# Optimization experiments

Hardware: AMD Instinct MI355X
Metric: run time of the kernel (lower is better)

Reference implementation:

```python
import jax, jax.numpy as jnp
import numpy as np

B, N, C, D, UP, KNN, MULT, PH = 4, 2048, 256, 64, 4, 20, 4, 64
EPS = 1e-5


def conv1d(x, w, b):
    # x: (B, Cin, N), w: (Cout, Cin)
    return jnp.einsum('oc,bcn->bon', w, x) + b[None, :, None]


def conv2d(x, w, b):
    # x: (B, Cin, N, K), 1x1 conv
    return jnp.einsum('oc,bcnk->bonk', w, x) + b[None, :, None, None]


def bn2d(x, g, bt, rm, rv):
    # eval-mode BatchNorm2d with running stats
    inv = jax.lax.rsqrt(rv + EPS)
    return g[None, :, None, None] * (x - rm[None, :, None, None]) * inv[None, :, None, None] + bt[None, :, None, None]


def group(f, idx):
    # f: (B, C, N), idx: (B, N, K) -> (B, C, N, K)
    return jax.vmap(lambda fb, ib: fb[:, ib])(f, idx)


def setup_inputs() -> dict:
    k0 = jax.random.key(0)
    ks = iter(jax.random.split(k0, 48))
    nx = lambda: next(ks)
    rn = lambda shape, s=0.05: jax.random.normal(nx(), shape, dtype=jnp.float32) * s
    z = lambda n: jnp.zeros((n,), jnp.float32)
    o = lambda n: jnp.ones((n,), jnp.float32)
    inp = {
        'pos': jax.random.normal(nx(), (B, 3, N), dtype=jnp.float32),
        'key': jax.random.normal(nx(), (B, C, N), dtype=jnp.float32),
        'query': jax.random.normal(nx(), (B, C, N), dtype=jnp.float32),
        # MLP_Res (mlp_v): in_dim=2C, hidden=C, out=C
        'wv1': rn((C, 2 * C)), 'bv1': z(C),
        'wv2': rn((C, C)), 'bv2': z(C),
        'wvs': rn((C, 2 * C)), 'bvs': z(C),
        # key/query/value projections to dim D
        'wk': rn((D, C)), 'bk': z(D),
        'wq': rn((D, C)), 'bq': z(D),
        'wval': rn((D, C)), 'bval': z(D),
        # pos_mlp: Conv2d(3,PH) -> BN -> ReLU -> Conv2d(PH,D)
        'pw1': rn((PH, 3)), 'pb1': z(PH), 'pg': o(PH), 'pbt': z(PH), 'prm': z(PH), 'prv': o(PH),
        'pw2': rn((D, PH)), 'pb2': z(D),
        # attn_mlp: Conv2d(D, D*MULT) -> BN -> ReLU -> ConvTranspose2d(D*MULT, D, (UP,1), (UP,1))
        'aw1': rn((D * MULT, D)), 'ab1': z(D * MULT), 'ag': o(D * MULT), 'abt': z(D * MULT), 'arm': z(D * MULT), 'arv': o(D * MULT),
        'ctw': rn((D * MULT, D, UP)), 'ctb': z(D),
        # conv_end: Conv1d(D, C)
        'we': rn((C, D)), 'be': z(C),
    }
    return inp


def reference(pos, key, query, wv1, bv1, wv2, bv2, wvs, bvs, wk, bk, wq, bq, wval, bval,
              pw1, pb1, pg, pbt, prm, prv, pw2, pb2,
              aw1, ab1, ag, abt, arm, arv, ctw, ctb, we, be):
    # mlp_v (MLP_Res) on concat([key, query])
    x = jnp.concatenate([key, query], axis=1)  # (B, 2C, N)
    value = conv1d(jax.nn.relu(conv1d(x, wv1, bv1)), wv2, bv2) + conv1d(x, wvs, bvs)  # (B, C, N)
    identity = value

    k_f = conv1d(key, wk, bk)      # (B, D, N)
    q_f = conv1d(query, wq, bq)    # (B, D, N)
    v_f = conv1d(value, wval, bval)

    # KNN (include_self=True): smallest-KNN indices of pairwise sq distance
    p = jnp.transpose(pos, (0, 2, 1))  # (B, N, 3)
    sq = jnp.sum(p * p, axis=-1)
    dist = sq[:, :, None] + sq[:, None, :] - 2.0 * jnp.einsum('bnc,bmc->bnm', p, p)
    idx = jax.lax.top_k(-dist, KNN)[1]  # (B, N, KNN)

    k_g = group(k_f, idx)                              # (B, D, N, KNN)
    qk_rel = q_f[:, :, :, None] - k_g
    pos_rel = pos[:, :, :, None] - group(pos, idx)     # (B, 3, N, KNN)

    h = jax.nn.relu(bn2d(conv2d(pos_rel, pw1, pb1), pg, pbt, prm, prv))
    pos_emb = conv2d(h, pw2, pb2)                      # (B, D, N, KNN)

    a = jax.nn.relu(bn2d(conv2d(qk_rel + pos_emb, aw1, ab1), ag, abt, arm, arv))  # (B, D*MULT, N, KNN)
    # ConvTranspose2d with kernel=(UP,1), stride=(UP,1): non-overlapping, out[b,o,n*UP+r,k]
    ct = jnp.einsum('bcnk,cor->bornk', a, ctw)         # (B, D, UP, N, KNN)
    Bv = a.shape[0]
    ct = jnp.transpose(ct, (0, 1, 3, 2, 4)).reshape(Bv, D, N * UP, KNN) + ctb[None, :, None, None]
    attn = jax.nn.softmax(ct, axis=-1)                 # softmax over neighbors

    v_g = group(v_f, idx) + pos_emb                    # (B, D, N, KNN)
    v_up = jnp.repeat(v_g, UP, axis=2)                 # nearest Upsample (UP,1)
    agg = jnp.sum(attn * v_up, axis=-1)                # (B, D, N*UP)
    y = conv1d(agg, we, be)                            # (B, C, N*UP)
    return y + jnp.repeat(identity, UP, axis=2)
```

## Files before the change

kernel.cpp:

```cpp
#include <hip/hip_runtime.h>
#include <hip/hip_bf16.h>

#define Bq 4
#define Nq 2048
#define Cq 256
#define Dq 64
#define UPq 4
#define KNNq 20
#define PHq 64
#define DMq 256
#define PTS 16

typedef __attribute__((ext_vector_type(8))) short short8;
typedef __attribute__((ext_vector_type(4))) short short4v;
typedef __attribute__((ext_vector_type(4))) float f32x4;
typedef __hip_bfloat16 bf16;

__device__ __forceinline__ void ld16(float* d, const float* s){
  *reinterpret_cast<float4*>(d) = *reinterpret_cast<const float4*>(s);
}
__device__ __forceinline__ unsigned short f2b(float x){
  bf16 h = __float2bfloat16(x);
  return *reinterpret_cast<unsigned short*>(&h);
}
__device__ __forceinline__ float b2f(short s){
  return __bfloat162float(*reinterpret_cast<bf16*>(&s));
}

__device__ __forceinline__ void swz(const float* __restrict__ src,
                                    short* __restrict__ dst,
                                    int M, int K, int g, bool transp)
{
  int j = g & 7, lane = (g >> 3) & 63, rest = g >> 9;
  int KS = K >> 5;
  int ks = rest % KS, mt = rest / KS;
  int m = mt*16 + (lane & 15);
  int k = ks*32 + ((lane >> 4) << 3) + j;
  float v = transp ? src[k*M + m] : src[m*K + k];
  dst[g] = (short)f2b(v);
}

__device__ __forceinline__ void swz_s(const float* __restrict__ src,
                                      short* __restrict__ dst,
                                      int M, int K, int g,
                                      const float* __restrict__ gam,
                                      const float* __restrict__ var)
{
  int j = g & 7, lane = (g >> 3) & 63, rest = g >> 9;
  int KS = K >> 5;
  int ks = rest % KS, mt = rest / KS;
  int m = mt*16 + (lane & 15);
  int k = ks*32 + ((lane >> 4) << 3) + j;
  float sc = gam[m] * rsqrtf(var[m] + 1e-5f);
  dst[g] = (short)f2b(src[m*K + k] * sc);
}

__global__ __launch_bounds__(256) void k_prep(
    const float* __restrict__ aw1, const float* __restrict__ ctw,
    const float* __restrict__ wv1, const float* __restrict__ wvs,
    const float* __restrict__ wv2, const float* __restrict__ wk,
    const float* __restrict__ wq,  const float* __restrict__ wval,
    const float* __restrict__ pw2, const float* __restrict__ we,
    short* __restrict__ aw1b, short* __restrict__ ctwT,
    short* __restrict__ wv1b, short* __restrict__ wvsb,
    short* __restrict__ wv2b, short* __restrict__ wkb,
    short* __restrict__ wqb,  short* __restrict__ wvalb,
    short* __restrict__ pw2b, short* __restrict__ web,
    const float* __restrict__ ag, const float* __restrict__ arv)
{
  const int t = threadIdx.x, bidx = blockIdx.x;
  if (bidx < 512){
    swz(wv1, wv1b, 256, 512, bidx*256 + t, false);
  } else if (bidx < 1024){
    swz(wvs, wvsb, 256, 512, (bidx-512)*256 + t, false);
  } else if (bidx < 1280){
    swz(wv2, wv2b, 256, 256, (bidx-1024)*256 + t, false);
  } else if (bidx < 1344){
    swz(wk, wkb, 64, 256, (bidx-1280)*256 + t, false);
  } else if (bidx < 1408){
    swz(wq, wqb, 64, 256, (bidx-1344)*256 + t, false);
  } else if (bidx < 1472){
    swz(wval, wvalb, 64, 256, (bidx-1408)*256 + t, false);
  } else if (bidx < 1488){
    swz(pw2, pw2b, 64, 64, (bidx-1472)*256 + t, false);
  } else if (bidx < 1552){
    swz_s(aw1, aw1b, 256, 64, (bidx-1488)*256 + t, ag, arv);
  } else if (bidx < 1616){
    swz(we, web, 256, 64, (bidx-1552)*256 + t, false);
  } else {
    swz(ctw, ctwT, 256, 256, (bidx-1616)*256 + t, true);
  }
}

__global__ __launch_bounds__(256) void k_value(
    const float* __restrict__ key, const float* __restrict__ query,
    const short* __restrict__ wv1b, const short* __restrict__ wvsb,
    const short* __restrict__ wv2b, const short* __restrict__ wkb,
    const short* __restrict__ wqb,  const short* __restrict__ wvalb,
    const float* __restrict__ bv1, const float* __restrict__ bv2,
    const float* __restrict__ bvs, const float* __restrict__ bk,
    const float* __restrict__ bq,  const float* __restrict__ bval,
    float* __restrict__ valueT, short* __restrict__ kfT,
    short* __restrict__ qfT,    short* __restrict__ vfT)
{
  __shared__ __align__(16) short Xb[16*520];
  __shared__ __align__(16) short hidB[16*264];
  __shared__ __align__(16) short valB[16*264];
  __shared__ __align__(16) float valF[16*264];
  const int t = threadIdx.x;
  const int b = blockIdx.x >> 7;
  const int n0 = (blockIdx.x & 127) * PTS;
  const int lane = t & 63, quad = lane >> 4, l15 = lane & 15, w = t >> 6;

  {
    const int c4 = t >> 2, pq = t & 3;
    #pragma unroll
    for (int pass=0; pass<4; pass++){
      int c = pass*64 + c4;
      float4 kv = *reinterpret_cast<const float4*>(key   + ((size_t)(b*Cq+c))*Nq + n0 + pq*4);
      float4 qv = *reinterpret_cast<const float4*>(query + ((size_t)(b*Cq+c))*Nq + n0 + pq*4);
      const float* kf_ = (const float*)&kv;
      const float* qf_ = (const float*)&qv;
      #pragma unroll
      for (int i=0;i<4;i++){
        Xb[(pq*4+i)*520 + c]       = (short)f2b(kf_[i]);
        Xb[(pq*4+i)*520 + 256 + c] = (short)f2b(qf_[i]);
      }
    }
  }
  __syncthreads();

  f32x4 acc1[4], accS[4];
  #pragma unroll
  for (int jm=0;jm<4;jm++){ acc1[jm]=(f32x4)0.f; accS[jm]=(f32x4)0.f; }

  #pragma unroll
  for (int ks=0;ks<16;ks++){
    const int kcol = ks*32 + quad*8;
    short8 xb = *reinterpret_cast<const short8*>(&Xb[l15*520 + kcol]);
    #pragma unroll
    for (int jm=0;jm<4;jm++){
      int mt = w*4 + jm;
      short8 a1 = *reinterpret_cast<const short8*>(wv1b + ((mt*16+ks)*64 + lane)*8);
      short8 as = *reinterpret_cast<const short8*>(wvsb + ((mt*16+ks)*64 + lane)*8);
      acc1[jm] = __builtin_amdgcn_mfma_f32_16x16x32_bf16(a1, xb, acc1[jm], 0,0,0);
      accS[jm] = __builtin_amdgcn_mfma_f32_16x16x32_bf16(as, xb, accS[jm], 0,0,0);
    }
  }
  #pragma unroll
  for (int jm=0;jm<4;jm++){
    #pragma unroll
    for (int r=0;r<4;r++){
      int h = (w*4+jm)*16 + quad*4 + r;
      hidB[l15*264 + h] = (short)f2b(fmaxf(acc1[jm][r] + bv1[h], 0.f));
    }
  }
  __syncthreads();

  #pragma unroll
  for (int ks=0;ks<8;ks++){
    const int kcol = ks*32 + quad*8;
    short8 hb = *reinterpret_cast<const short8*>(&hidB[l15*264 + kcol]);
    #pragma unroll
    for (int jm=0;jm<4;jm++){
      int mt = w*4 + jm;
      short8 a = *reinterpret_cast<const short8*>(wv2b + ((mt*8+ks)*64 + lane)*8);
      accS[jm] = __builtin_amdgcn_mfma_f32_16x16x32_bf16(a, hb, accS[jm], 0,0,0);
    }
  }
  #pragma unroll
  for (int jm=0;jm<4;jm++){
    #pragma unroll
    for (int r=0;r<4;r++){
      int c = (w*4+jm)*16 + quad*4 + r;
      float v = accS[jm][r] + bv2[c] + bvs[c];
      valF[l15*264 + c] = v;
      valB[l15*264 + c] = (short)f2b(v);
    }
  }
  __syncthreads();

  #pragma unroll
  for (int p=0;p<PTS;p++)
    valueT[((size_t)(b*Nq + n0 + p))*Cq + t] = valF[p*264 + t];

  {
    f32x4 pk4=(f32x4)0.f, pq4=(f32x4)0.f, pv4=(f32x4)0.f;
    #pragma unroll
    for (int ks=0;ks<8;ks++){
      const int kcol = ks*32 + quad*8;
      short8 xk = *reinterpret_cast<const short8*>(&Xb[l15*520 + kcol]);
      short8 xq = *reinterpret_cast<const short8*>(&Xb[l15*520 + 256 + kcol]);
      short8 xv = *reinterpret_cast<const short8*>(&valB[l15*264 + kcol]);
      short8 ak = *reinterpret_cast<const short8*>(wkb  + ((w*8+ks)*64 + lane)*8);
      short8 aq = *reinterpret_cast<const short8*>(wqb  + ((w*8+ks)*64 + lane)*8);
      short8 av = *reinterpret_cast<const short8*>(wvalb+ ((w*8+ks)*64 + lane)*8);
      pk4 = __builtin_amdgcn_mfma_f32_16x16x32_bf16(ak, xk, pk4, 0,0,0);
      pq4 = __builtin_amdgcn_mfma_f32_16x16x32_bf16(aq, xq, pq4, 0,0,0);
      pv4 = __builtin_amdgcn_mfma_f32_16x16x32_bf16(av, xv, pv4, 0,0,0);
    }
    short4v ok, oq, ov;
    #pragma unroll
    for (int r=0;r<4;r++){
      int o = w*16 + quad*4 + r;
      ok[r] = (short)f2b(pk4[r] + bk[o]);
      oq[r] = (short)f2b(pq4[r] + bq[o]);
      ov[r] = (short)f2b(pv4[r] + bval[o]);
    }
    int n = n0 + l15;
    size_t base = ((size_t)(b*Nq+n))*Dq + w*16 + quad*4;
    *reinterpret_cast<short4v*>(kfT + base) = ok;
    *reinterpret_cast<short4v*>(qfT + base) = oq;
    *reinterpret_cast<short4v*>(vfT + base) = ov;
  }
}

__global__ __launch_bounds__(256) void k_knn(const float* __restrict__ pos,
                                             int* __restrict__ idxT)
{
  const int t = threadIdx.x;
  const int lane = t & 63;
  const int w = t >> 6;
  const int pid = blockIdx.x*4 + w;
  const int b = pid >> 11;
  const int n = pid & (Nq-1);
  const float* px = pos + (size_t)(b*3+0)*Nq;
  const float* py = pos + (size_t)(b*3+1)*Nq;
  const float* pz = pos + (size_t)(b*3+2)*Nq;
  const float xn=px[n], yn=py[n], zn=pz[n];
  const float sqn = __fadd_rn(__fadd_rn(__fmul_rn(xn,xn),__fmul_rn(yn,yn)),__fmul_rn(zn,zn));

  double kd[32];
  #pragma unroll
  for (int i=0;i<32;i++){
    int j = i*64 + lane;
    float x=px[j], y=py[j], z=pz[j];
    float sqj = __fadd_rn(__fadd_rn(__fmul_rn(x,x),__fmul_rn(y,y)),__fmul_rn(z,z));
    float dot = __fadd_rn(__fadd_rn(__fmul_rn(xn,x),__fmul_rn(yn,y)),__fmul_rn(zn,z));
    float d   = __fsub_rn(__fadd_rn(sqn,sqj), __fmul_rn(2.0f,dot));
    unsigned u = __float_as_uint(d);
    u ^= ((unsigned)((int)u >> 31)) | 0x80000000u;
    kd[i] = (double)u * 2048.0 + (double)j;
  }

  const double BIG = 9.0e15;
  double last = -1.0;
  for (int s=0;s<KNNq;s++){
    double c[16];
    #pragma unroll
    for (int i=0;i<16;i++){
      double a0 = (kd[i]    > last) ? kd[i]    : BIG;
      double a1 = (kd[i+16] > last) ? kd[i+16] : BIG;
      c[i] = fmin(a0, a1);
    }
    #pragma unroll
    for (int off=8; off>0; off>>=1){
      #pragma unroll
      for (int i=0;i<off;i++) c[i] = fmin(c[i], c[i+off]);
    }
    double m = c[0];
    #pragma unroll
    for (int off=1; off<64; off<<=1)
      m = fmin(m, __shfl_xor(m, off));
    if (lane == 0){
      unsigned long long kk = (unsigned long long)m;
      idxT[(size_t)pid*KNNq + s] = (int)(kk & 2047ull);
    }
    last = m;
  }
}

#define UADDR(row, colb) ((((row)*128 + (colb)) ^ (((row)&7)<<4)))
#define SADDR(row, colb) ((((row)*256 + (colb)) ^ (((row)&7)<<4)))

__global__ __launch_bounds__(256, 4) void k_attn(
  const float* __restrict__ pos,
  const float* __restrict__ valueT, const short* __restrict__ kfT,
  const short* __restrict__ qfT,    const short* __restrict__ vfT,
  const int* __restrict__ idxT,
  const float* __restrict__ pw1, const float* __restrict__ pb1,
  const float* __restrict__ pg,  const float* __restrict__ pbt,
  const float* __restrict__ prm, const float* __restrict__ prv,
  const short* __restrict__ pw2b, const float* __restrict__ pb2,
  const short* __restrict__ aw1b, const float* __restrict__ ab1,
  const float* __restrict__ ag,  const float* __restrict__ abt,
  const float* __restrict__ arm, const float* __restrict__ arv,
  const short* __restrict__ ctwT,
  const short* __restrict__ web,  const float* __restrict__ be,
  float* __restrict__ out)
{
  __shared__ __align__(16) char unionA[22528];
  __shared__ __align__(16) char unionB[6144];
  __shared__ __align__(16) char unionC[6144];
  __shared__ __align__(16) short vgB[64*40];

  float* sh2S = (float*)(unionA + 12288);
  float* prl  = (float*)unionC;
  int*   nb   = (int*)(unionC + 576);

  const int t = threadIdx.x;
  const int b  = blockIdx.x >> 10;
  const int n0 = (blockIdx.x & 1023) * 2;
  const int lane = t & 63, quad = lane >> 4, l15 = lane & 15, w = t >> 6;
  const size_t bN = (size_t)b * Nq;
  const int obase = w*16 + quad*4;

  if (t < 48){
    int p = (t >= 24);
    int k = t - p*24;
    int nn = n0 + p;
    int j = (k < KNNq) ? idxT[(bN + nn)*KNNq + k] : nn;
    nb[t] = j;
    #pragma unroll
    for (int d=0; d<3; d++){
      prl[d*48+t] = pos[((size_t)(b*3+d))*Nq + nn] - pos[((size_t)(b*3+d))*Nq + j];
    }
  }
  {
    float sc = ag[t] * rsqrtf(arv[t] + 1e-5f);
    sh2S[t]  = ab1[t]*sc + (abt[t] - arm[t]*sc);
  }
  __syncthreads();

  short4v pq4[3], pk4[3], pv4[3];
  #pragma unroll
  for (int nt=0; nt<3; nt++){
    int pk = nt*16 + l15;
    int p  = (pk >= 24);
    int j  = nb[pk];
    pq4[nt] = *reinterpret_cast<const short4v*>(qfT + (bN + n0 + p)*Dq + obase);
    pk4[nt] = *reinterpret_cast<const short4v*>(kfT + (bN + j)*Dq + obase);
    pv4[nt] = *reinterpret_cast<const short4v*>(vfT + (bN + j)*Dq + obase);
  }

  {
    const int ph = t & 63;
    float sc = pg[ph] * rsqrtf(prv[ph] + 1e-5f);
    float w0 = pw1[ph*3+0]*sc, w1 = pw1[ph*3+1]*sc, w2 = pw1[ph*3+2]*sc;
    float bb = pb1[ph]*sc + (pbt[ph] - prm[ph]*sc);
    #pragma unroll
    for (int m=0;m<12;m++){
      int pk = w + m*4;
      float h = fmaf(w0, prl[pk], fmaf(w1, prl[48+pk], fmaf(w2, prl[96+pk], bb)));
      *(short*)(unionB + UADDR(pk, ph*2)) = (short)f2b(fmaxf(h, 0.f));
    }
  }
  __syncthreads();

  {
    f32x4 accP[3];
    #pragma unroll
    for (int nt=0;nt<3;nt++) accP[nt]=(f32x4)0.f;
    #pragma unroll
    for (int ks=0;ks<2;ks++){
      const int kcolb = (ks*32 + quad*8)*2;
      short8 a = *reinterpret_cast<const short8*>(pw2b + ((w*2+ks)*64 + lane)*8);
      #pragma unroll
      for (int nt=0;nt<3;nt++){
        short8 bb = *reinterpret_cast<const short8*>(unionB + UADDR(nt*16+l15, kcolb));
        accP[nt] = __builtin_amdgcn_mfma_f32_16x16x32_bf16(a, bb, accP[nt], 0,0,0);
      }
    }
    #pragma unroll
    for (int nt=0;nt<3;nt++){
      int pk = nt*16 + l15;
      bool vld = (pk < 20) || (pk >= 24 && pk < 44);
      int col  = pk - (pk >= 24 ? 4 : 0);
      short4v ut4;
      #pragma unroll
      for (int r=0;r<4;r++){
        int o = obase + r;
        float pe = accP[nt][r] + pb2[o];
        ut4[r] = (short)f2b((b2f(pq4[nt][r]) - b2f(pk4[nt][r])) + pe);
        if (vld) vgB[o*40 + col] = (short)f2b(b2f(pv4[nt][r]) + pe);
      }
      *(short4v*)(unionC + UADDR(pk, obase*2)) = ut4;
    }
  }
  __syncthreads();

  f32x4 accT[4][3];
  #pragma unroll
  for (int jm=0;jm<4;jm++)
    #pragma unroll
    for (int nt=0;nt<3;nt++) accT[jm][nt]=(f32x4)0.f;

  #pragma unroll
  for (int ch=0; ch<2; ch++){
    f32x4 accC[2][3];
    #pragma unroll
    for (int jm=0;jm<2;jm++)
      #pragma unroll
      for (int nt=0;nt<3;nt++) accC[jm][nt]=(f32x4)0.f;
    #pragma unroll
    for (int ks=0;ks<2;ks++){
      const int kcolb = (ks*32 + quad*8)*2;
      short8 bb[3];
      #pragma unroll
      for (int nt=0;nt<3;nt++)
        bb[nt] = *reinterpret_cast<const short8*>(unionC + UADDR(nt*16+l15, kcolb));
      #pragma unroll
      for (int jm=0;jm<2;jm++){
        int mt = ch*8 + w*2 + jm;
        short8 a = *reinterpret_cast<const short8*>(aw1b + ((mt*2+ks)*64 + lane)*8);
        #pragma unroll
        for (int nt=0;nt<3;nt++)
          accC[jm][nt] = __builtin_amdgcn_mfma_f32_16x16x32_bf16(a, bb[nt], accC[jm][nt], 0,0,0);
      }
    }
    if (ch == 1) __syncthreads();
    #pragma unroll
    for (int jm=0;jm<2;jm++){
      const int colb = ((w*2+jm)*16 + quad*4)*2;
      #pragma unroll
      for (int nt=0;nt<3;nt++){
        int pk = nt*16 + l15;
        short4v pkv;
        #pragma unroll
        for (int r=0;r<4;r++){
          int c = ch*128 + (w*2+jm)*16 + quad*4 + r;
          pkv[r] = (short)f2b(fmaxf(accC[jm][nt][r] + sh2S[c], 0.f));
        }
        *(short4v*)(unionA + SADDR(pk, colb)) = pkv;
      }
    }
    __syncthreads();
    #pragma unroll
    for (int ksl=0; ksl<4; ksl++){
      const int kcolb = (ksl*32 + quad*8)*2;
      short8 bb[3];
      #pragma unroll
      for (int nt=0;nt<3;nt++)
        bb[nt] = *reinterpret_cast<const short8*>(unionA + SADDR(nt*16+l15, kcolb));
      #pragma unroll
      for (int jm=0;jm<4;jm++){
        int mt = w*4 + jm;
        short8 a = *reinterpret_cast<const short8*>(ctwT + ((mt*8 + ch*4 + ksl)*64 + lane)*8);
        #pragma unroll
        for (int nt=0;nt<3;nt++)
          accT[jm][nt] = __builtin_amdgcn_mfma_f32_16x16x32_bf16(a, bb[nt], accT[jm][nt], 0,0,0);
      }
    }
  }
  __syncthreads();

  #pragma unroll
  for (int nt=0;nt<3;nt++){
    int pk = nt*16 + l15;
    bool vld = (pk < 20) || (pk >= 24 && pk < 44);
    int col  = pk - (pk >= 24 ? 4 : 0);
    if (vld){
      #pragma unroll
      for (int jm=0;jm<4;jm++){
        #pragma unroll
        for (int r=0;r<4;r++){
          int row = (w*4+jm)*16 + quad*4 + r;
          *(short*)(unionA + row*88 + col*2) = (short)f2b(accT[jm][nt][r]);
        }
      }
    }
  }
  __syncthreads();

  float4 idv[4];
  if (l15 < 8){
    int p = l15 >> 2;
    #pragma unroll
    for (int jm=0;jm<4;jm++)
      idv[jm] = *reinterpret_cast<const float4*>(valueT + (bN + n0 + p)*Cq + (w*4+jm)*16 + quad*4);
  }
  {
    const int o = t >> 2, rr = t & 3;
    #pragma unroll
    for (int p=0;p<2;p++){
      float ct[20];
      #pragma unroll
      for (int q=0;q<5;q++){
        short4v cv = *reinterpret_cast<const short4v*>(unionA + t*88 + p*40 + q*8);
        #pragma unroll
        for (int i=0;i<4;i++) ct[q*4+i] = b2f(cv[i]);
      }
      float m = ct[0];
      #pragma unroll
      for (int k=1;k<20;k++) m = fmaxf(m, ct[k]);
      float s = 0.f, a = 0.f;
      #pragma unroll
      for (int q=0;q<5;q++){
        short4v vv = *reinterpret_cast<const short4v*>((const char*)vgB + o*80 + p*40 + q*8);
        #pragma unroll
        for (int i=0;i<4;i++){
          float e = __expf(ct[q*4+i] - m);
          s += e;
          a = fmaf(e, b2f(vv[i]), a);
        }
      }
      *(short*)(unionB + UADDR(p*4+rr, o*2)) = (short)f2b(__fdividef(a, s));
    }
  }
  __syncthreads();

  {
    f32x4 accE[4];
    #pragma unroll
    for (int jm=0;jm<4;jm++) accE[jm]=(f32x4)0.f;
    #pragma unroll
    for (int ks=0;ks<2;ks++){
      const int kcolb = (ks*32 + quad*8)*2;
      short8 bb = *reinterpret_cast<const short8*>(unionB + UADDR(l15, kcolb));
      #pragma unroll
      for (int jm=0;jm<4;jm++){
        int mt = w*4 + jm;
        short8 a = *reinterpret_cast<const short8*>(web + ((mt*2+ks)*64 + lane)*8);
        accE[jm] = __builtin_amdgcn_mfma_f32_16x16x32_bf16(a, bb, accE[jm], 0,0,0);
      }
    }
    if (l15 < 8){
      int p = l15 >> 2, rr = l15 & 3;
      #pragma unroll
      for (int jm=0;jm<4;jm++){
        float4 b4 = *reinterpret_cast<const float4*>(be + (w*4+jm)*16 + quad*4);
        #pragma unroll
        for (int r=0;r<4;r++){
          int c = (w*4+jm)*16 + quad*4 + r;
          float y = accE[jm][r] + ((const float*)&b4)[r] + ((const float*)&idv[jm])[r];
          out[((size_t)(b*Cq+c))*((size_t)Nq*UPq) + (size_t)(n0+p)*UPq + rr] = y;
        }
      }
    }
  }
}

extern "C" void kernel_launch(void* const* d_in, const int* in_sizes, int n_in,
                              void* d_out, int out_size, void* d_ws, size_t ws_size,
                              hipStream_t stream)
{
  const float* pos  = (const float*)d_in[0];
  const float* key  = (const float*)d_in[1];
  const float* qry  = (const float*)d_in[2];
  const float* wv1  = (const float*)d_in[3];
  const float* bv1  = (const float*)d_in[4];
  const float* wv2  = (const float*)d_in[5];
  const float* bv2  = (const float*)d_in[6];
  const float* wvs  = (const float*)d_in[7];
  const float* bvs  = (const float*)d_in[8];
  const float* wk   = (const float*)d_in[9];
  const float* bk   = (const float*)d_in[10];
  const float* wq   = (const float*)d_in[11];
  const float* bq   = (const float*)d_in[12];
  const float* wval = (const float*)d_in[13];
  const float* bval = (const float*)d_in[14];
  const float* pw1  = (const float*)d_in[15];
  const float* pb1  = (const float*)d_in[16];
  const float* pg   = (const float*)d_in[17];
  const float* pbt  = (const float*)d_in[18];
  const float* prm  = (const float*)d_in[19];
  const float* prv  = (const float*)d_in[20];
  const float* pw2  = (const float*)d_in[21];
  const float* pb2  = (const float*)d_in[22];
  const float* aw1  = (const float*)d_in[23];
  const float* ab1  = (const float*)d_in[24];
  const float* ag   = (const float*)d_in[25];
  const float* abt  = (const float*)d_in[26];
  const float* arm  = (const float*)d_in[27];
  const float* arv  = (const float*)d_in[28];
  const float* ctw  = (const float*)d_in[29];
  const float* we   = (const float*)d_in[31];
  const float* be   = (const float*)d_in[32];

  char* ws = (char*)d_ws;
  float* valueT = (float*)(ws);
  short* kfT    = (short*)(ws + 8388608);
  short* qfT    = (short*)(ws + 9437184);
  short* vfT    = (short*)(ws + 10485760);
  int*   idxT   = (int*)  (ws + 11534336);
  short* aw1b   = (short*)(ws + 12189696);
  short* ctwT   = (short*)(ws + 12222464);
  short* wv1b   = (short*)(ws + 12353536);
  short* wvsb   = (short*)(ws + 12615680);
  short* wv2b   = (short*)(ws + 12877824);
  short* wkb    = (short*)(ws + 13008896);
  short* wqb    = (short*)(ws + 13041664);
  short* wvalb  = (short*)(ws + 13074432);
  short* pw2b   = (short*)(ws + 13107200);
  short* web    = (short*)(ws + 13115392);
  float* out    = (float*)d_out;

  k_prep<<<dim3(1872), dim3(256), 0, stream>>>(
      aw1, ctw, wv1, wvs, wv2, wk, wq, wval, pw2, we,
      aw1b, ctwT, wv1b, wvsb, wv2b, wkb, wqb, wvalb, pw2b, web,
      ag, arv);
  k_value<<<dim3(Bq*Nq/PTS), dim3(256), 0, stream>>>(
      key, qry, wv1b, wvsb, wv2b, wkb, wqb, wvalb,
      bv1, bv2, bvs, bk, bq, bval,
      valueT, kfT, qfT, vfT);
  k_knn<<<dim3(Bq*Nq/4), dim3(256), 0, stream>>>(pos, idxT);
  k_attn<<<dim3(Bq*Nq/2), dim3(256), 0, stream>>>(
      pos, valueT, kfT, qfT, vfT, idxT,
      pw1, pb1, pg, pbt, prm, prv, pw2b, pb2,
      aw1b, ab1, ag, abt, arm, arv, ctwT, web, be, out);
}
```

Before: 285.3 us.

## Process four points per attention block with 512 threads to widen MFMA tiles

The attention kernel now handles four query points per block with eight waves instead of two points with four waves. Shared buffers double in size and the warp-to-tile mapping changes so each wave covers six neighbor tiles in the attn_mlp GEMMs. This is meant to reuse each loaded weight fragment across more neighbor columns and to halve the block count. The cost is more shared memory and registers per block, which can lower occupancy, and a launch_bounds of (512,4) that may be hard to satisfy.

```diff
diff --git a/kernel.cpp b/kernel.cpp
--- a/kernel.cpp
+++ b/kernel.cpp
@@ -16,9 +16,6 @@
 typedef __attribute__((ext_vector_type(4))) float f32x4;
 typedef __hip_bfloat16 bf16;
 
-__device__ __forceinline__ void ld16(float* d, const float* s){
-  *reinterpret_cast<float4*>(d) = *reinterpret_cast<const float4*>(s);
-}
 __device__ __forceinline__ unsigned short f2b(float x){
   bf16 h = __float2bfloat16(x);
   return *reinterpret_cast<unsigned short*>(&h);
@@ -273,7 +270,7 @@
 #define UADDR(row, colb) ((((row)*128 + (colb)) ^ (((row)&7)<<4)))
 #define SADDR(row, colb) ((((row)*256 + (colb)) ^ (((row)&7)<<4)))
 
-__global__ __launch_bounds__(256, 4) void k_attn(
+__global__ __launch_bounds__(512, 4) void k_attn(
   const float* __restrict__ pos,
   const float* __restrict__ valueT, const short* __restrict__ kfT,
   const short* __restrict__ qfT,    const short* __restrict__ vfT,
@@ -289,34 +286,36 @@
   const short* __restrict__ web,  const float* __restrict__ be,
   float* __restrict__ out)
 {
-  __shared__ __align__(16) char unionA[22528];
-  __shared__ __align__(16) char unionB[6144];
-  __shared__ __align__(16) char unionC[6144];
-  __shared__ __align__(16) short vgB[64*40];
-
-  float* sh2S = (float*)(unionA + 12288);
+  __shared__ __align__(16) char unionA[43008];
+  __shared__ __align__(16) char unionB[12288];
+  __shared__ __align__(16) char unionC[12288];
+  __shared__ __align__(16) short vgB[64*84];
+
+  float* sh2S = (float*)(unionA + 24576);
   float* prl  = (float*)unionC;
-  int*   nb   = (int*)(unionC + 576);
+  int*   nb   = (int*)(unionC + 1152);
 
   const int t = threadIdx.x;
-  const int b  = blockIdx.x >> 10;
-  const int n0 = (blockIdx.x & 1023) * 2;
+  const int b  = blockIdx.x >> 9;
+  const int n0 = (blockIdx.x & 511) * 4;
   const int lane = t & 63, quad = lane >> 4, l15 = lane & 15, w = t >> 6;
   const size_t bN = (size_t)b * Nq;
-  const int obase = w*16 + quad*4;
-
-  if (t < 48){
-    int p = (t >= 24);
+  const int wm = w & 3;
+  const int ntb = (w >> 2) * 3;
+  const int obase2 = wm*16 + quad*4;
+
+  if (t < 96){
+    int p = (t*683) >> 14;
     int k = t - p*24;
     int nn = n0 + p;
     int j = (k < KNNq) ? idxT[(bN + nn)*KNNq + k] : nn;
     nb[t] = j;
     #pragma unroll
     for (int d=0; d<3; d++){
-      prl[d*48+t] = pos[((size_t)(b*3+d))*Nq + nn] - pos[((size_t)(b*3+d))*Nq + j];
-    }
-  }
-  {
+      prl[d*96+t] = pos[((size_t)(b*3+d))*Nq + nn] - pos[((size_t)(b*3+d))*Nq + j];
+    }
+  }
+  if (t < 256){
     float sc = ag[t] * rsqrtf(arv[t] + 1e-5f);
     sh2S[t]  = ab1[t]*sc + (abt[t] - arm[t]*sc);
   }
@@ -325,12 +324,12 @@
   short4v pq4[3], pk4[3], pv4[3];
   #pragma unroll
   for (int nt=0; nt<3; nt++){
-    int pk = nt*16 + l15;
-    int p  = (pk >= 24);
+    int pk = (ntb+nt)*16 + l15;
+    int p  = (pk*683) >> 14;
     int j  = nb[pk];
-    pq4[nt] = *reinterpret_cast<const short4v*>(qfT + (bN + n0 + p)*Dq + obase);
-    pk4[nt] = *reinterpret_cast<const short4v*>(kfT + (bN + j)*Dq + obase);
-    pv4[nt] = *reinterpret_cast<const short4v*>(vfT + (bN + j)*Dq + obase);
+    pq4[nt] = *reinterpret_cast<const short4v*>(qfT + (bN + n0 + p)*Dq + obase2);
+    pk4[nt] = *reinterpret_cast<const short4v*>(kfT + (bN + j)*Dq + obase2);
+    pv4[nt] = *reinterpret_cast<const short4v*>(vfT + (bN + j)*Dq + obase2);
   }
 
   {
@@ -340,8 +339,8 @@
     float bb = pb1[ph]*sc + (pbt[ph] - prm[ph]*sc);
     #pragma unroll
     for (int m=0;m<12;m++){
-      int pk = w + m*4;
-      float h = fmaf(w0, prl[pk], fmaf(w1, prl[48+pk], fmaf(w2, prl[96+pk], bb)));
+      int pk = w + m*8;
+      float h = fmaf(w0, prl[pk], fmaf(w1, prl[96+pk], fmaf(w2, prl[192+pk], bb)));
       *(short*)(unionB + UADDR(pk, ph*2)) = (short)f2b(fmaxf(h, 0.f));
     }
   }
@@ -354,72 +353,65 @@
     #pragma unroll
     for (int ks=0;ks<2;ks++){
       const int kcolb = (ks*32 + quad*8)*2;
-      short8 a = *reinterpret_cast<const short8*>(pw2b + ((w*2+ks)*64 + lane)*8);
+      short8 a = *reinterpret_cast<const short8*>(pw2b + ((wm*2+ks)*64 + lane)*8);
       #pragma unroll
       for (int nt=0;nt<3;nt++){
-        short8 bb = *reinterpret_cast<const short8*>(unionB + UADDR(nt*16+l15, kcolb));
+        short8 bb = *reinterpret_cast<const short8*>(unionB + UADDR((ntb+nt)*16+l15, kcolb));
         accP[nt] = __builtin_amdgcn_mfma_f32_16x16x32_bf16(a, bb, accP[nt], 0,0,0);
       }
     }
     #pragma unroll
     for (int nt=0;nt<3;nt++){
-      int pk = nt*16 + l15;
-      bool vld = (pk < 20) || (pk >= 24 && pk < 44);
-      int col  = pk - (pk >= 24 ? 4 : 0);
+      int pk = (ntb+nt)*16 + l15;
+      int p  = (pk*683) >> 14;
+      int k  = pk - p*24;
+      bool vld = (k < KNNq);
+      int col  = p*20 + k;
       short4v ut4;
       #pragma unroll
       for (int r=0;r<4;r++){
-        int o = obase + r;
+        int o = obase2 + r;
         float pe = accP[nt][r] + pb2[o];
         ut4[r] = (short)f2b((b2f(pq4[nt][r]) - b2f(pk4[nt][r])) + pe);
-        if (vld) vgB[o*40 + col] = (short)f2b(b2f(pv4[nt][r]) + pe);
-      }
-      *(short4v*)(unionC + UADDR(pk, obase*2)) = ut4;
-    }
-  }
-  __syncthreads();
-
-  f32x4 accT[4][3];
-  #pragma unroll
-  for (int jm=0;jm<4;jm++)
-    #pragma unroll
-    for (int nt=0;nt<3;nt++) accT[jm][nt]=(f32x4)0.f;
+        if (vld) vgB[o*84 + col] = (short)f2b(b2f(pv4[nt][r]) + pe);
+      }
+      *(short4v*)(unionC + UADDR(pk, obase2*2)) = ut4;
+    }
+  }
+  __syncthreads();
+
+  f32x4 accT[2][6];
+  #pragma unroll
+  for (int jm=0;jm<2;jm++)
+    #pragma unroll
+    for (int nt=0;nt<6;nt++) accT[jm][nt]=(f32x4)0.f;
 
   #pragma unroll
   for (int ch=0; ch<2; ch++){
-    f32x4 accC[2][3];
-    #pragma unroll
-    for (int jm=0;jm<2;jm++)
-      #pragma unroll
-      for (int nt=0;nt<3;nt++) accC[jm][nt]=(f32x4)0.f;
+    f32x4 accC[6];
+    #pragma unroll
+    for (int nt=0;nt<6;nt++) accC[nt]=(f32x4)0.f;
     #pragma unroll
     for (int ks=0;ks<2;ks++){
       const int kcolb = (ks*32 + quad*8)*2;
-      short8 bb[3];
-      #pragma unroll
-      for (int nt=0;nt<3;nt++)
-        bb[nt] = *reinterpret_cast<const short8*>(unionC + UADDR(nt*16+l15, kcolb));
-      #pragma unroll
-      for (int jm=0;jm<2;jm++){
-        int mt = ch*8 + w*2 + jm;
-        short8 a = *reinterpret_cast<const short8*>(aw1b + ((mt*2+ks)*64 + lane)*8);
-        #pragma unroll
-        for (int nt=0;nt<3;nt++)
-          accC[jm][nt] = __builtin_amdgcn_mfma_f32_16x16x32_bf16(a, bb[nt], accC[jm][nt], 0,0,0);
+      short8 a = *reinterpret_cast<const short8*>(aw1b + (((ch*8+w)*2+ks)*64 + lane)*8);
+      #pragma unroll
+      for (int nt=0;nt<6;nt++){
+        short8 bb = *reinterpret_cast<const short8*>(unionC + UADDR(nt*16+l15, kcolb));
+        accC[nt] = __builtin_amdgcn_mfma_f32_16x16x32_bf16(a, bb, accC[nt], 0,0,0);
       }
     }
     if (ch == 1) __syncthreads();
-    #pragma unroll
-    for (int jm=0;jm<2;jm++){
-      const int colb = ((w*2+jm)*16 + quad*4)*2;
-      #pragma unroll
-      for (int nt=0;nt<3;nt++){
+    {
+      const int colb = (w*16 + quad*4)*2;
+      #pragma unroll
+      for (int nt=0;nt<6;nt++){
         int pk = nt*16 + l15;
         short4v pkv;
         #pragma unroll
         for (int r=0;r<4;r++){
-          int c = ch*128 + (w*2+jm)*16 + quad*4 + r;
-          pkv[r] = (short)f2b(fmaxf(accC[jm][nt][r] + sh2S[c], 0.f));
+          int c = ch*128 + w*16 + quad*4 + r;
+          pkv[r] = (short)f2b(fmaxf(accC[nt][r] + sh2S[c], 0.f));
         }
         *(short4v*)(unionA + SADDR(pk, colb)) = pkv;
       }
@@ -428,55 +420,58 @@
     #pragma unroll
     for (int ksl=0; ksl<4; ksl++){
       const int kcolb = (ksl*32 + quad*8)*2;
-      short8 bb[3];
-      #pragma unroll
-      for (int nt=0;nt<3;nt++)
-        bb[nt] = *reinterpret_cast<const short8*>(unionA + SADDR(nt*16+l15, kcolb));
-      #pragma unroll
-      for (int jm=0;jm<4;jm++){
-        int mt = w*4 + jm;
+      short8 bb6[6];
+      #pragma unroll
+      for (int nt=0;nt<6;nt++)
+        bb6[nt] = *reinterpret_cast<const short8*>(unionA + SADDR(nt*16+l15, kcolb));
+      #pragma unroll
+      for (int jm=0;jm<2;jm++){
+        int mt = w*2 + jm;
         short8 a = *reinterpret_cast<const short8*>(ctwT + ((mt*8 + ch*4 + ksl)*64 + lane)*8);
         #pragma unroll
-        for (int nt=0;nt<3;nt++)
-          accT[jm][nt] = __builtin_amdgcn_mfma_f32_16x16x32_bf16(a, bb[nt], accT[jm][nt], 0,0,0);
-      }
-    }
-  }
-  __syncthreads();
-
-  #pragma unroll
-  for (int nt=0;nt<3;nt++){
+        for (int nt=0;nt<6;nt++)
+          accT[jm][nt] = __builtin_amdgcn_mfma_f32_16x16x32_bf16(a, bb6[nt], accT[jm][nt], 0,0,0);
+      }
+    }
+  }
+  __syncthreads();
+
+  #pragma unroll
+  for (int nt=0;nt<6;nt++){
     int pk = nt*16 + l15;
-    bool vld = (pk < 20) || (pk >= 24 && pk < 44);
-    int col  = pk - (pk >= 24 ? 4 : 0);
-    if (vld){
-      #pragma unroll
-      for (int jm=0;jm<4;jm++){
+    int p  = (pk*683) >> 14;
+    int k  = pk - p*24;
+    if (k < KNNq){
+      int col = p*20 + k;
+      #pragma unroll
+      for (int jm=0;jm<2;jm++){
         #pragma unroll
         for (int r=0;r<4;r++){
-          int row = (w*4+jm)*16 + quad*4 + r;
-          *(short*)(unionA + row*88 + col*2) = (short)f2b(accT[jm][nt][r]);
+          int row = (w*2+jm)*16 + quad*4 + r;
+          *(short*)(unionA + row*168 + col*2) = (short)f2b(accT[jm][nt][r]);
         }
       }
     }
   }
   __syncthreads();
 
-  float4 idv[4];
-  if (l15 < 8){
+  float4 idv[2];
+  {
     int p = l15 >> 2;
     #pragma unroll
-    for (int jm=0;jm<4;jm++)
-      idv[jm] = *reinterpret_cast<const float4*>(valueT + (bN + n0 + p)*Cq + (w*4+jm)*16 + quad*4);
-  }
-  {
-    const int o = t >> 2, rr = t & 3;
-    #pragma unroll
-    for (int p=0;p<2;p++){
+    for (int jm=0;jm<2;jm++)
+      idv[jm] = *reinterpret_cast<const float4*>(valueT + (bN + n0 + p)*Cq + (w*2+jm)*16 + quad*4);
+  }
+  {
+    const int row = t & 255, phh = t >> 8;
+    const int o = row >> 2, rr = row & 3;
+    #pragma unroll
+    for (int pp=0;pp<2;pp++){
+      int p = phh*2 + pp;
       float ct[20];
       #pragma unroll
       for (int q=0;q<5;q++){
-        short4v cv = *reinterpret_cast<const short4v*>(unionA + t*88 + p*40 + q*8);
+        short4v cv = *reinterpret_cast<const short4v*>(unionA + row*168 + p*40 + q*8);
         #pragma unroll
         for (int i=0;i<4;i++) ct[q*4+i] = b2f(cv[i]);
       }
@@ -486,7 +481,7 @@
       float s = 0.f, a = 0.f;
       #pragma unroll
       for (int q=0;q<5;q++){
-        short4v vv = *reinterpret_cast<const short4v*>((const char*)vgB + o*80 + p*40 + q*8);
+        short4v vv = *reinterpret_cast<const short4v*>((const char*)vgB + o*168 + p*40 + q*8);
         #pragma unroll
         for (int i=0;i<4;i++){
           float e = __expf(ct[q*4+i] - m);
@@ -500,28 +495,28 @@
   __syncthreads();
 
   {
-    f32x4 accE[4];
-    #pragma unroll
-    for (int jm=0;jm<4;jm++) accE[jm]=(f32x4)0.f;
+    f32x4 accE[2];
+    #pragma unroll
+    for (int jm=0;jm<2;jm++) accE[jm]=(f32x4)0.f;
     #pragma unroll
     for (int ks=0;ks<2;ks++){
       const int kcolb = (ks*32 + quad*8)*2;
       short8 bb = *reinterpret_cast<const short8*>(unionB + UADDR(l15, kcolb));
       #pragma unroll
-      for (int jm=0;jm<4;jm++){
-        int mt = w*4 + jm;
+      for (int jm=0;jm<2;jm++){
+        int mt = w*2 + jm;
         short8 a = *reinterpret_cast<const short8*>(web + ((mt*2+ks)*64 + lane)*8);
         accE[jm] = __builtin_amdgcn_mfma_f32_16x16x32_bf16(a, bb, accE[jm], 0,0,0);
       }
     }
-    if (l15 < 8){
+    {
       int p = l15 >> 2, rr = l15 & 3;
       #pragma unroll
-      for (int jm=0;jm<4;jm++){
-        float4 b4 = *reinterpret_cast<const float4*>(be + (w*4+jm)*16 + quad*4);
+      for (int jm=0;jm<2;jm++){
+        float4 b4 = *reinterpret_cast<const float4*>(be + (w*2+jm)*16 + quad*4);
         #pragma unroll
         for (int r=0;r<4;r++){
-          int c = (w*4+jm)*16 + quad*4 + r;
+          int c = (w*2+jm)*16 + quad*4 + r;
           float y = accE[jm][r] + ((const float*)&b4)[r] + ((const float*)&idv[jm])[r];
           out[((size_t)(b*Cq+c))*((size_t)Nq*UPq) + (size_t)(n0+p)*UPq + rr] = y;
         }
@@ -594,7 +589,7 @@
       bv1, bv2, bvs, bk, bq, bval,
       valueT, kfT, qfT, vfT);
   k_knn<<<dim3(Bq*Nq/4), dim3(256), 0, stream>>>(pos, idxT);
-  k_attn<<<dim3(Bq*Nq/2), dim3(256), 0, stream>>>(
+  k_attn<<<dim3(Bq*Nq/4), dim3(512), 0, stream>>>(
       pos, valueT, kfT, qfT, vfT, idxT,
       pw1, pb1, pg, pbt, prm, prv, pw2b, pb2,
       aw1b, ab1, ag, abt, arm, arv, ctwT, web, be, out);
```

Result: slower. 299.7 us (+5.1%).
